# Kernel tuning notes

Hardware: AMD Instinct MI355X
Metric: run time of the kernel (lower is better)

Reference implementation:

```python
import jax, jax.numpy as jnp
import numpy as np

N = 50000        # nodes
E = 400000       # edges (avg degree 8)
F_IN = 128       # num_features
HID = 64         # hidden_channels
H = 4            # num_heads
D = HID // H     # headc = 16
C = 16           # num_classes
K_HOPS = 3
ALPHA = 0.1
CST = 1e-5


def setup_inputs() -> dict:
    key = jax.random.key(0)
    ks = jax.random.split(key, 16)
    s = 0.05
    x = jax.random.normal(ks[0], (N, F_IN), dtype=jnp.float32)
    edge_index = jax.random.randint(ks[1], (2, E), 0, N, dtype=jnp.int64)
    Wi = jax.random.normal(ks[2], (F_IN, HID), dtype=jnp.float32) * s
    bi = jnp.zeros((HID,), dtype=jnp.float32)
    Wq = jax.random.normal(ks[3], (HID, H * D), dtype=jnp.float32) * s
    bq = jnp.zeros((H * D,), dtype=jnp.float32)
    Wk = jax.random.normal(ks[4], (HID, H * D), dtype=jnp.float32) * s
    bk = jnp.zeros((H * D,), dtype=jnp.float32)
    Wv = jax.random.normal(ks[5], (HID, H * C), dtype=jnp.float32) * s
    bv = jnp.zeros((H * C,), dtype=jnp.float32)
    Wo = jax.random.normal(ks[6], (H * C, C), dtype=jnp.float32) * s
    bo = jnp.zeros((C,), dtype=jnp.float32)
    # hopwise/temp init as in the torch module (ind_gamma=True, gamma_softmax=True)
    hw = ALPHA * (1.0 - ALPHA) ** np.arange(K_HOPS + 1)
    hw[-1] = (1.0 - ALPHA) ** K_HOPS
    hopwise = jnp.asarray(hw, dtype=jnp.float32)
    temp = jax.random.uniform(ks[7], (H, K_HOPS + 1), dtype=jnp.float32)
    return {"x": x, "edge_index": edge_index, "Wi": Wi, "bi": bi, "Wq": Wq,
            "bq": bq, "Wk": Wk, "bk": bk, "Wv": Wv, "bv": bv, "Wo": Wo,
            "bo": bo, "hopwise": hopwise, "temp": temp}


def reference(x, edge_index, Wi, bi, Wq, bq, Wk, bk, Wv, bv, Wo, bo, hopwise, temp):
    # dropout p=0 (inference); input transform + relu
    h = jax.nn.relu(x @ Wi + bi)                       # (N, HID)
    Q = (1.0 + jax.nn.elu(h @ Wq + bq)).reshape(N, H, D)
    Kt = (1.0 + jax.nn.elu(h @ Wk + bk)).reshape(N, H, D)
    V = (h @ Wv + bv).reshape(N, H, C)
    M = jnp.einsum('nhi,nhj->nhij', Kt, V)             # (N, H, D, C)
    hidden = V * temp[:, 0][None, :, None]             # hop-0 term
    # NB: torch F.softmax(temp, dim=-2) normalizes over the HEAD axis
    layerwise = jax.nn.softmax(temp, axis=0)           # (H, K+1)
    src, dst = edge_index[0], edge_index[1]
    for hop in range(K_HOPS):
        M = jax.ops.segment_sum(M[src], dst, num_segments=N)
        Kt = jax.ops.segment_sum(Kt[src], dst, num_segments=N)
        Hm = jnp.einsum('nhi,nhij->nhj', Q, M)         # (N, H, C)
        den = jnp.einsum('nhi,nhi->nh', Q, Kt)[..., None] + CST
        gamma = hopwise[hop + 1] * layerwise[:, hop + 1][:, None]  # (H, 1)
        hidden = hidden + gamma * (Hm / den)
    # multi_concat=True path
    out = hidden.reshape(N, H * C) @ Wo + bo           # (N, C)
    return out
```

## Files before the change

kernel.cpp:

```cpp
#include <hip/hip_runtime.h>
#include <math.h>

#define F_IN 128
#define HID  64
#define NH   4
#define DD   16
#define CC   16
#define CSTE 1e-5f

typedef _Float16 h2     __attribute__((ext_vector_type(2)));
typedef float    f2     __attribute__((ext_vector_type(2)));
typedef short    short8 __attribute__((ext_vector_type(8)));
typedef float    f4v    __attribute__((ext_vector_type(4)));

#define WIT_LD 136
#define W2T_LD 72
#define H_LD   72

__device__ __forceinline__ unsigned short bf16r(float f) {
    unsigned int u = __builtin_bit_cast(unsigned int, f);
    unsigned int r = (u + 0x7FFFu + ((u >> 16) & 1u)) >> 16;
    return (unsigned short)r;
}

__device__ __forceinline__ float fp8_to_f32(unsigned int b) {
    f2 v = __builtin_amdgcn_cvt_pk_f32_fp8((int)b, false);
    return v.x;
}
__device__ __forceinline__ f2 fp8x2_to_f32(unsigned int w) {
    return __builtin_amdgcn_cvt_pk_f32_fp8((int)w, false);
}
__device__ __forceinline__ unsigned char f32_to_fp8(float f) {
    int w = __builtin_amdgcn_cvt_pk_fp8_f32(f, f, 0, false);
    return (unsigned char)(w & 0xff);
}

__device__ __forceinline__ float fp4_dec1(unsigned int n) {
    unsigned int e = (n >> 1) & 3u, m = n & 1u;
    float mag = (e == 0) ? 0.5f * (float)m
                         : (float)(1u << (e - 1)) * (1.0f + 0.5f * (float)m);
    return (n & 8u) ? -mag : mag;
}
__device__ __forceinline__ unsigned int fp4_enc1(float f) {
    unsigned int s = (f < 0.f) ? 8u : 0u;
    float a = fabsf(f);
    unsigned int m;
    if      (a < 0.25f) m = 0u;
    else if (a < 0.75f) m = 1u;
    else if (a < 1.25f) m = 2u;
    else if (a < 1.75f) m = 3u;
    else if (a < 2.5f)  m = 4u;
    else if (a < 3.5f)  m = 5u;
    else if (a < 5.0f)  m = 6u;
    else                m = 7u;
    return s | m;
}

#if __has_builtin(__builtin_amdgcn_cvt_scalef32_pk_f32_fp4) && __has_builtin(__builtin_amdgcn_cvt_scalef32_pk_fp4_f32)
#define HAS_FP4 1
#endif

__device__ __forceinline__ void fp4x16_dec(uint2 w, float* v) {
#ifdef HAS_FP4
    f2 r;
    r = __builtin_amdgcn_cvt_scalef32_pk_f32_fp4(w.x, 1.0f, 0); v[0]  = r.x; v[1]  = r.y;
    r = __builtin_amdgcn_cvt_scalef32_pk_f32_fp4(w.x, 1.0f, 1); v[2]  = r.x; v[3]  = r.y;
    r = __builtin_amdgcn_cvt_scalef32_pk_f32_fp4(w.x, 1.0f, 2); v[4]  = r.x; v[5]  = r.y;
    r = __builtin_amdgcn_cvt_scalef32_pk_f32_fp4(w.x, 1.0f, 3); v[6]  = r.x; v[7]  = r.y;
    r = __builtin_amdgcn_cvt_scalef32_pk_f32_fp4(w.y, 1.0f, 0); v[8]  = r.x; v[9]  = r.y;
    r = __builtin_amdgcn_cvt_scalef32_pk_f32_fp4(w.y, 1.0f, 1); v[10] = r.x; v[11] = r.y;
    r = __builtin_amdgcn_cvt_scalef32_pk_f32_fp4(w.y, 1.0f, 2); v[12] = r.x; v[13] = r.y;
    r = __builtin_amdgcn_cvt_scalef32_pk_f32_fp4(w.y, 1.0f, 3); v[14] = r.x; v[15] = r.y;
#else
    #pragma unroll
    for (int j = 0; j < 8; ++j) {
        v[j]     = fp4_dec1((w.x >> (4 * j)) & 0xFu);
        v[8 + j] = fp4_dec1((w.y >> (4 * j)) & 0xFu);
    }
#endif
}

__device__ __forceinline__ uint2 fp4x16_enc(const float* v) {
#ifdef HAS_FP4
    unsigned int a = 0u, b = 0u;
    a = __builtin_amdgcn_cvt_scalef32_pk_fp4_f32(a, v[0],  v[1],  1.0f, 0);
    a = __builtin_amdgcn_cvt_scalef32_pk_fp4_f32(a, v[2],  v[3],  1.0f, 1);
    a = __builtin_amdgcn_cvt_scalef32_pk_fp4_f32(a, v[4],  v[5],  1.0f, 2);
    a = __builtin_amdgcn_cvt_scalef32_pk_fp4_f32(a, v[6],  v[7],  1.0f, 3);
    b = __builtin_amdgcn_cvt_scalef32_pk_fp4_f32(b, v[8],  v[9],  1.0f, 0);
    b = __builtin_amdgcn_cvt_scalef32_pk_fp4_f32(b, v[10], v[11], 1.0f, 1);
    b = __builtin_amdgcn_cvt_scalef32_pk_fp4_f32(b, v[12], v[13], 1.0f, 2);
    b = __builtin_amdgcn_cvt_scalef32_pk_fp4_f32(b, v[14], v[15], 1.0f, 3);
    return {a, b};
#else
    unsigned int a = 0u, b = 0u;
    #pragma unroll
    for (int j = 0; j < 8; ++j) {
        a |= fp4_enc1(v[j])     << (4 * j);
        b |= fp4_enc1(v[8 + j]) << (4 * j);
    }
    return {a, b};
#endif
}

__device__ __forceinline__ void store_m_row(
    uint2* __restrict__ Mout, unsigned short* __restrict__ SKout,
    int node, int lane, const float* u, float kacc)
{
    float rm = 0.f;
    #pragma unroll
    for (int j = 0; j < 16; ++j) rm = fmaxf(rm, fabsf(u[j]));
    unsigned char s8 = f32_to_fp8(rm * (1.0f / 6.0f));
    float se = fp8_to_f32((unsigned int)s8);
    float invs = (se > 0.f) ? (1.0f / se) : 0.f;
    float tq[16];
    #pragma unroll
    for (int j = 0; j < 16; ++j) tq[j] = u[j] * invs;
    Mout[(size_t)node * 64 + lane] = fp4x16_enc(tq);
    SKout[(size_t)node * 64 + lane] =
        (unsigned short)((unsigned short)s8 | ((unsigned short)f32_to_fp8(kacc) << 8));
}

__device__ __forceinline__ float gamma_for(const float* __restrict__ temp,
                                           const float* __restrict__ hopwise,
                                           int h, int hop) {
    float t0 = temp[0 * 4 + hop], t1 = temp[1 * 4 + hop];
    float t2 = temp[2 * 4 + hop], t3 = temp[3 * 4 + hop];
    float mx = fmaxf(fmaxf(t0, t1), fmaxf(t2, t3));
    float e0 = __expf(t0 - mx), e1 = __expf(t1 - mx);
    float e2 = __expf(t2 - mx), e3 = __expf(t3 - mx);
    float ssum = e0 + e1 + e2 + e3;
    float eh = (h == 0) ? e0 : (h == 1) ? e1 : (h == 2) ? e2 : e3;
    return hopwise[hop] * eh / ssum;
}

__device__ __forceinline__ void reduce_scatter16(float* u, int p) {
    #pragma unroll
    for (int k = 0; k < 4; ++k) {
        const int m = 1 << k;
        bool bit = (p >> k) & 1;
        const int n = 8 >> k;
        #pragma unroll
        for (int j = 0; j < n; ++j) {
            float give = bit ? u[2 * j]     : u[2 * j + 1];
            float keep = bit ? u[2 * j + 1] : u[2 * j];
            float got  = __shfl_xor(give, m, 64);
            u[j] = keep + got;
        }
    }
}

__device__ __forceinline__ float den16(float qd, float kacc) {
    float kq = qd * kacc;
    kq += __shfl_xor(kq, 1, 64);
    kq += __shfl_xor(kq, 2, 64);
    kq += __shfl_xor(kq, 4, 64);
    kq += __shfl_xor(kq, 8, 64);
    return kq + CSTE;
}

__global__ __launch_bounds__(1024) void scan_a(const int* __restrict__ deg,
                                               int* __restrict__ offsets,
                                               int* __restrict__ bsum, int N) {
    __shared__ int wsum[16], woff[16];
    int lane = threadIdx.x & 63, w = threadIdx.x >> 6;
    int i0 = blockIdx.x * 4096 + (int)threadIdx.x * 4;
    int d0 = (i0 + 0 < N) ? deg[i0 + 0] : 0;
    int d1 = (i0 + 1 < N) ? deg[i0 + 1] : 0;
    int d2 = (i0 + 2 < N) ? deg[i0 + 2] : 0;
    int d3 = (i0 + 3 < N) ? deg[i0 + 3] : 0;
    int tsum = d0 + d1 + d2 + d3;
    int incl = tsum;
    #pragma unroll
    for (int m = 1; m < 64; m <<= 1) {
        int t = __shfl_up(incl, m, 64);
        if (lane >= m) incl += t;
    }
    if (lane == 63) wsum[w] = incl;
    __syncthreads();
    if (threadIdx.x == 0) {
        int r = 0;
        for (int k = 0; k < 16; ++k) { int t = wsum[k]; woff[k] = r; r += t; }
        bsum[blockIdx.x] = r;
    }
    __syncthreads();
    int excl = woff[w] + incl - tsum;
    if (i0 + 0 < N) offsets[i0 + 0] = excl;
    if (i0 + 1 < N) offsets[i0 + 1] = excl + d0;
    if (i0 + 2 < N) offsets[i0 + 2] = excl + d0 + d1;
    if (i0 + 3 < N) offsets[i0 + 3] = excl + d0 + d1 + d2;
}

__global__ void scan_c(int* __restrict__ offsets, const int* __restrict__ bsum,
                       int nb, int N) {
    int i = blockIdx.x * blockDim.x + threadIdx.x;
    if (i < N) {
        int bkt = i >> 12;
        int base = 0;
        for (int b = 0; b < bkt; ++b) base += bsum[b];
        offsets[i] += base;
    }
    if (i == 0) {
        int tot = 0;
        for (int b = 0; b < nb; ++b) tot += bsum[b];
        offsets[N] = tot;
    }
}

__global__ void scatter_kernel(const int* __restrict__ ei, const int* __restrict__ offsets,
                               int* __restrict__ cursor, int* __restrict__ csr, int E) {
    int e = blockIdx.x * blockDim.x + threadIdx.x;
    if (e < E) {
        int src = ei[e];
        int dst = ei[E + e];
        int pos = atomicAdd(&cursor[dst], 1);
        csr[offsets[dst] + pos] = src;
    }
}

__global__ __launch_bounds__(256) void qkv_count(
    const float* __restrict__ x,
    const float* __restrict__ Wi, const float* __restrict__ bi,
    const float* __restrict__ Wq, const float* __restrict__ bq,
    const float* __restrict__ Wk, const float* __restrict__ bk,
    const float* __restrict__ Wv, const float* __restrict__ bv,
    const float* __restrict__ temp,
    float* __restrict__ Q, unsigned char* __restrict__ K0,
    _Float16* __restrict__ Vh, float* __restrict__ hidden,
    const int* __restrict__ ei, int* __restrict__ deg,
    int E, int qb, int N)
{
    __shared__ unsigned short wit[64 * WIT_LD];
    __shared__ unsigned short w2t[192 * W2T_LD];
    __shared__ unsigned short hlds[64 * H_LD];
    if ((int)blockIdx.x >= qb) {
        int e = ((int)blockIdx.x - qb) * 256 + (int)threadIdx.x;
        if (e < E) atomicAdd(&deg[ei[E + e]], 1);
        return;
    }
    int t = threadIdx.x;
    #pragma unroll
    for (int i = 0; i < 32; ++i) {
        int g = t + i * 256;
        wit[(g & 63) * WIT_LD + (g >> 6)] = bf16r(Wi[g]);
    }
    #pragma unroll
    for (int i = 0; i < 16; ++i) {
        int g = t + i * 256;
        int k = g >> 6, n = g & 63;
        w2t[(n      ) * W2T_LD + k] = bf16r(Wq[g]);
        w2t[(n +  64) * W2T_LD + k] = bf16r(Wk[g]);
        w2t[(n + 128) * W2T_LD + k] = bf16r(Wv[g]);
    }
    __syncthreads();

    int lane = t & 63, w = t >> 6;
    int p = lane & 15, quad = lane >> 4;
    int mbase = blockIdx.x * 64 + w * 16;

    short8 afrag[4];
    {
        int node = mbase + p;
        if (node >= N) node = N - 1;
        const float* xr = x + (size_t)node * F_IN + quad * 8;
        #pragma unroll
        for (int ks = 0; ks < 4; ++ks) {
            float4 a0 = *(const float4*)(xr + ks * 32);
            float4 a1 = *(const float4*)(xr + ks * 32 + 4);
            short8 f;
            f[0] = bf16r(a0.x); f[1] = bf16r(a0.y); f[2] = bf16r(a0.z); f[3] = bf16r(a0.w);
            f[4] = bf16r(a1.x); f[5] = bf16r(a1.y); f[6] = bf16r(a1.z); f[7] = bf16r(a1.w);
            afrag[ks] = f;
        }
    }
    #pragma unroll
    for (int nt = 0; nt < 4; ++nt) {
        f4v acc = {0.f, 0.f, 0.f, 0.f};
        #pragma unroll
        for (int ks = 0; ks < 4; ++ks) {
            short8 b = *(const short8*)&wit[(nt * 16 + p) * WIT_LD + ks * 32 + quad * 8];
            acc = __builtin_amdgcn_mfma_f32_16x16x32_bf16(afrag[ks], b, acc, 0, 0, 0);
        }
        float bb = bi[nt * 16 + p];
        #pragma unroll
        for (int r = 0; r < 4; ++r) {
            float hv = fmaxf(acc[r] + bb, 0.f);
            hlds[(w * 16 + quad * 4 + r) * H_LD + nt * 16 + p] = bf16r(hv);
        }
    }
    __syncthreads();

    short8 ha0 = *(const short8*)&hlds[(w * 16 + p) * H_LD + quad * 8];
    short8 ha1 = *(const short8*)&hlds[(w * 16 + p) * H_LD + 32 + quad * 8];
    int node_r = mbase + quad * 4;
    #pragma unroll
    for (int nt = 0; nt < 12; ++nt) {
        f4v acc = {0.f, 0.f, 0.f, 0.f};
        short8 b0 = *(const short8*)&w2t[(nt * 16 + p) * W2T_LD + quad * 8];
        short8 b1 = *(const short8*)&w2t[(nt * 16 + p) * W2T_LD + 32 + quad * 8];
        acc = __builtin_amdgcn_mfma_f32_16x16x32_bf16(ha0, b0, acc, 0, 0, 0);
        acc = __builtin_amdgcn_mfma_f32_16x16x32_bf16(ha1, b1, acc, 0, 0, 0);
        int col = nt * 16 + p;
        #pragma unroll
        for (int r = 0; r < 4; ++r) {
            int node = node_r + r;
            if (node >= N) continue;
            float v = acc[r];
            if (col < 64) {
                v += bq[col];
                Q[(size_t)node * 64 + col] = (v > 0.f) ? (1.f + v) : __expf(v);
            } else if (col < 128) {
                int c = col - 64;
                v += bk[c];
                float kv = (v > 0.f) ? (1.f + v) : __expf(v);
                K0[(size_t)node * 64 + c] = f32_to_fp8(kv);
            } else {
                int c = col - 128;
                v += bv[c];
                Vh[(size_t)node * 64 + c] = (_Float16)v;
                hidden[(size_t)node * 64 + c] = v * temp[(c >> 4) * 4];
            }
        }
    }
}


__global__ __launch_bounds__(256) void hop1_all(
    const float* __restrict__ Q, const unsigned char* __restrict__ K0,
    const _Float16* __restrict__ Vh,
    const int* __restrict__ offsets, const int* __restrict__ csr,
    const float* __restrict__ temp, const float* __restrict__ hopwise,
    uint2* __restrict__ M1, unsigned short* __restrict__ SK1,
    float* __restrict__ hidden, int N)
{
    int lane = threadIdx.x & 63;
    int node = blockIdx.x * 4 + (threadIdx.x >> 6);
    if (node >= N) return;
    int h = lane >> 4;
    float gh = gamma_for(temp, hopwise, h, 1);
    h2 u16[8];
    #pragma unroll
    for (int j = 0; j < 8; ++j) u16[j] = h2{(_Float16)0.f, (_Float16)0.f};
    float kacc = 0.f;
    int beg = offsets[node], end = offsets[node + 1];
    int t = beg;
    for (; t + 1 < end; t += 2) {
        int s0 = csr[t], s1 = csr[t + 1];
        const uint4* v0p = (const uint4*)(Vh + (size_t)s0 * 64 + h * 16);
        const uint4* v1p = (const uint4*)(Vh + (size_t)s1 * 64 + h * 16);
        uint4 a0 = v0p[0], a1 = v0p[1];
        uint4 b0 = v1p[0], b1 = v1p[1];
        float k0 = fp8_to_f32(K0[(size_t)s0 * 64 + lane]);
        float k1 = fp8_to_f32(K0[(size_t)s1 * 64 + lane]);
        kacc += k0 + k1;
        _Float16 k0h = (_Float16)k0, k1h = (_Float16)k1;
        h2 k02 = {k0h, k0h}, k12 = {k1h, k1h};
        const unsigned int aw[8] = {a0.x, a0.y, a0.z, a0.w, a1.x, a1.y, a1.z, a1.w};
        const unsigned int bw[8] = {b0.x, b0.y, b0.z, b0.w, b1.x, b1.y, b1.z, b1.w};
        #pragma unroll
        for (int j = 0; j < 8; ++j) {
            u16[j] += k02 * __builtin_bit_cast(h2, aw[j]);
            u16[j] += k12 * __builtin_bit_cast(h2, bw[j]);
        }
    }
    for (; t < end; ++t) {
        int s = csr[t];
        const uint4* vp = (const uint4*)(Vh + (size_t)s * 64 + h * 16);
        uint4 a0 = vp[0], a1 = vp[1];
        float kk = fp8_to_f32(K0[(size_t)s * 64 + lane]);
        kacc += kk;
        _Float16 kh = (_Float16)kk;
        h2 k2 = {kh, kh};
        const unsigned int aw[8] = {a0.x, a0.y, a0.z, a0.w, a1.x, a1.y, a1.z, a1.w};
        #pragma unroll
        for (int j = 0; j < 8; ++j)
            u16[j] += k2 * __builtin_bit_cast(h2, aw[j]);
    }
    float u[16];
    #pragma unroll
    for (int j = 0; j < 8; ++j) { u[2 * j] = (float)u16[j].x; u[2 * j + 1] = (float)u16[j].y; }
    store_m_row(M1, SK1, node, lane, u, kacc);
    float qd = Q[(size_t)node * 64 + lane];
    #pragma unroll
    for (int j = 0; j < 16; ++j) u[j] *= qd;
    reduce_scatter16(u, lane & 15);
    float g = gh / den16(qd, kacc);
    hidden[(size_t)node * 64 + lane] += g * u[0];
}

template<bool STORE>
__global__ __launch_bounds__(256) void hop23_all(
    const float* __restrict__ Q, const uint2* __restrict__ Mprev,
    const unsigned short* __restrict__ SKprev,
    const int* __restrict__ offsets, const int* __restrict__ csr,
    const float* __restrict__ temp, const float* __restrict__ hopwise,
    uint2* __restrict__ Mnext, unsigned short* __restrict__ SKnext,
    float* __restrict__ hidden, int N, int hop)
{
    int lane = threadIdx.x & 63;
    int node = blockIdx.x * 4 + (threadIdx.x >> 6);
    if (node >= N) return;
    float gh = gamma_for(temp, hopwise, lane >> 4, hop);
    const uint2* Mb = Mprev + lane;
    const unsigned short* SKb = SKprev + lane;
    float u[16];
    #pragma unroll
    for (int j = 0; j < 16; ++j) u[j] = 0.f;
    float kacc = 0.f;
    int beg = offsets[node], end = offsets[node + 1];
    int t = beg;
    for (; t + 3 < end; t += 4) {
        int s0 = csr[t], s1 = csr[t + 1], s2 = csr[t + 2], s3 = csr[t + 3];
        uint2 w0 = Mb[(size_t)s0 * 64];
        uint2 w1 = Mb[(size_t)s1 * 64];
        uint2 w2 = Mb[(size_t)s2 * 64];
        uint2 w3 = Mb[(size_t)s3 * 64];
        f2 sk0 = fp8x2_to_f32(SKb[(size_t)s0 * 64]);
        f2 sk1 = fp8x2_to_f32(SKb[(size_t)s1 * 64]);
        f2 sk2 = fp8x2_to_f32(SKb[(size_t)s2 * 64]);
        f2 sk3 = fp8x2_to_f32(SKb[(size_t)s3 * 64]);
        kacc += (sk0.y + sk1.y) + (sk2.y + sk3.y);
        float v[16];
        fp4x16_dec(w0, v);
        #pragma unroll
        for (int j = 0; j < 16; ++j) u[j] = fmaf(sk0.x, v[j], u[j]);
        fp4x16_dec(w1, v);
        #pragma unroll
        for (int j = 0; j < 16; ++j) u[j] = fmaf(sk1.x, v[j], u[j]);
        fp4x16_dec(w2, v);
        #pragma unroll
        for (int j = 0; j < 16; ++j) u[j] = fmaf(sk2.x, v[j], u[j]);
        fp4x16_dec(w3, v);
        #pragma unroll
        for (int j = 0; j < 16; ++j) u[j] = fmaf(sk3.x, v[j], u[j]);
    }
    for (; t < end; ++t) {
        int sn = csr[t];
        uint2 w = Mb[(size_t)sn * 64];
        f2 sk = fp8x2_to_f32(SKb[(size_t)sn * 64]);
        kacc += sk.y;
        float v[16];
        fp4x16_dec(w, v);
        #pragma unroll
        for (int j = 0; j < 16; ++j) u[j] = fmaf(sk.x, v[j], u[j]);
    }
    if (STORE) store_m_row(Mnext, SKnext, node, lane, u, kacc);
    float qd = Q[(size_t)node * 64 + lane];
    #pragma unroll
    for (int j = 0; j < 16; ++j) u[j] *= qd;
    reduce_scatter16(u, lane & 15);
    float g = gh / den16(qd, kacc);
    hidden[(size_t)node * 64 + lane] += g * u[0];
}

__global__ __launch_bounds__(256) void out_kernel(
    const float* __restrict__ hidden, const float* __restrict__ Wo,
    const float* __restrict__ bo, float* __restrict__ out, int N)
{
    __shared__ float wo[HID * CC];
    for (int i = threadIdx.x; i < HID * CC; i += 256) wo[i] = Wo[i];
    __syncthreads();
    int idx = blockIdx.x * 256 + threadIdx.x;
    int n = idx >> 4, c = idx & 15;
    if (n >= N) return;
    float acc = bo[c];
    const float4* hp4 = (const float4*)(hidden + (size_t)n * HID);
    #pragma unroll
    for (int j4 = 0; j4 < 16; ++j4) {
        float4 hv = hp4[j4];
        acc += hv.x * wo[(4 * j4 + 0) * CC + c] + hv.y * wo[(4 * j4 + 1) * CC + c]
             + hv.z * wo[(4 * j4 + 2) * CC + c] + hv.w * wo[(4 * j4 + 3) * CC + c];
    }
    out[(size_t)n * CC + c] = acc;
}

extern "C" void kernel_launch(void* const* d_in, const int* in_sizes, int n_in,
                              void* d_out, int out_size, void* d_ws, size_t ws_size,
                              hipStream_t stream) {
    const float* x       = (const float*)d_in[0];
    const int*   ei      = (const int*)  d_in[1];
    const float* Wi      = (const float*)d_in[2];
    const float* bi      = (const float*)d_in[3];
    const float* Wq      = (const float*)d_in[4];
    const float* bq      = (const float*)d_in[5];
    const float* Wk      = (const float*)d_in[6];
    const float* bk      = (const float*)d_in[7];
    const float* Wv      = (const float*)d_in[8];
    const float* bv      = (const float*)d_in[9];
    const float* Wo      = (const float*)d_in[10];
    const float* bo      = (const float*)d_in[11];
    const float* hopwise = (const float*)d_in[12];
    const float* temp    = (const float*)d_in[13];

    const int N = in_sizes[0] / F_IN;
    const int E = in_sizes[1] / 2;

    char* ws = (char*)d_ws;
    size_t off = 0;
    auto take = [&](size_t bytes) -> char* {
        char* p = ws + off;
        off += (bytes + 255) & ~(size_t)255;
        return p;
    };
    float*          Q      = (float*)take((size_t)N * 64 * 4);
    _Float16*       Vh     = (_Float16*)take((size_t)N * 64 * 2);
    float*          hidden = (float*)take((size_t)N * 64 * 4);
    unsigned char*  K0     = (unsigned char*)take((size_t)N * 64);
    unsigned short* SK1    = (unsigned short*)take((size_t)N * 64 * 2);
    unsigned short* SK2    = (unsigned short*)take((size_t)N * 64 * 2);
    int*            degcur = (int*)take((size_t)2 * N * 4);
    int*            offs   = (int*)take((size_t)(N + 1) * 4);
    int*            csr    = (int*)take((size_t)E * 4);
    int             nb     = (N + 4095) / 4096;
    int*            bsum   = (int*)take((size_t)nb * 4);
    uint2*          M1     = (uint2*)take((size_t)N * 512);
    uint2*          M2     = (uint2*)take((size_t)N * 512);

    int* deg    = degcur;
    int* cursor = degcur + N;

    hipMemsetAsync(degcur, 0, (size_t)2 * N * 4, stream);

    int eb = (E + 255) / 256;
    int qb = (N + 63) / 64;
    qkv_count<<<qb + eb, 256, 0, stream>>>(x, Wi, bi, Wq, bq, Wk, bk, Wv, bv,
                                           temp, Q, K0, Vh, hidden,
                                           ei, deg, E, qb, N);
    scan_a<<<nb, 1024, 0, stream>>>(deg, offs, bsum, N);
    scan_c<<<(N + 255) / 256, 256, 0, stream>>>(offs, bsum, nb, N);
    scatter_kernel<<<eb, 256, 0, stream>>>(ei, offs, cursor, csr, E);

    int nb4 = (N + 3) / 4;
    hop1_all<<<nb4, 256, 0, stream>>>(Q, K0, Vh, offs, csr, temp, hopwise,
                                      M1, SK1, hidden, N);
    hop23_all<true ><<<nb4, 256, 0, stream>>>(Q, M1, SK1, offs, csr, temp, hopwise,
                                              M2, SK2, hidden, N, 2);
    hop23_all<false><<<nb4, 256, 0, stream>>>(Q, M2, SK2, offs, csr, temp, hopwise,
                                              (uint2*)nullptr, (unsigned short*)nullptr,
                                              hidden, N, 3);

    int ob = (N * CC + 255) / 256;
    out_kernel<<<ob, 256, 0, stream>>>(hidden, Wo, bo, (float*)d_out, N);
}
```

Baseline: 311.7 us.

## Fuse output projection into final hop and move hop-0 term into hop1

Removes the separate output-projection kernel by computing the hidden·Wo product inside the last hop kernel, using a per-lane Wo row and a cross-lane reduce. The hop-0 hidden initialization moves from the QKV kernel into hop1, which now writes hidden instead of read-modify-writing it. The hop2/3 inner accumulation switches to packed f32 FMA through inline asm, with paired fp4 decode. This saves one launch and several full passes over the hidden buffer, at the cost of more shuffles and registers in the final hop.

```diff
diff --git a/kernel.cpp b/kernel.cpp
--- a/kernel.cpp
+++ b/kernel.cpp
@@ -21,6 +21,11 @@
     unsigned int u = __builtin_bit_cast(unsigned int, f);
     unsigned int r = (u + 0x7FFFu + ((u >> 16) & 1u)) >> 16;
     return (unsigned short)r;
+}
+
+__device__ __forceinline__ f2 pk_fma(f2 a, f2 b, f2 c) {
+    asm("v_pk_fma_f32 %0, %1, %2, %0" : "+v"(c) : "v"(a), "v"(b));
+    return c;
 }
 
 __device__ __forceinline__ float fp8_to_f32(unsigned int b) {
@@ -60,22 +65,23 @@
 #define HAS_FP4 1
 #endif
 
-__device__ __forceinline__ void fp4x16_dec(uint2 w, float* v) {
+__device__ __forceinline__ void fp4x16_dec2(uint2 w, f2* v) {
 #ifdef HAS_FP4
-    f2 r;
-    r = __builtin_amdgcn_cvt_scalef32_pk_f32_fp4(w.x, 1.0f, 0); v[0]  = r.x; v[1]  = r.y;
-    r = __builtin_amdgcn_cvt_scalef32_pk_f32_fp4(w.x, 1.0f, 1); v[2]  = r.x; v[3]  = r.y;
-    r = __builtin_amdgcn_cvt_scalef32_pk_f32_fp4(w.x, 1.0f, 2); v[4]  = r.x; v[5]  = r.y;
-    r = __builtin_amdgcn_cvt_scalef32_pk_f32_fp4(w.x, 1.0f, 3); v[6]  = r.x; v[7]  = r.y;
-    r = __builtin_amdgcn_cvt_scalef32_pk_f32_fp4(w.y, 1.0f, 0); v[8]  = r.x; v[9]  = r.y;
-    r = __builtin_amdgcn_cvt_scalef32_pk_f32_fp4(w.y, 1.0f, 1); v[10] = r.x; v[11] = r.y;
-    r = __builtin_amdgcn_cvt_scalef32_pk_f32_fp4(w.y, 1.0f, 2); v[12] = r.x; v[13] = r.y;
-    r = __builtin_amdgcn_cvt_scalef32_pk_f32_fp4(w.y, 1.0f, 3); v[14] = r.x; v[15] = r.y;
+    v[0] = __builtin_amdgcn_cvt_scalef32_pk_f32_fp4(w.x, 1.0f, 0);
+    v[1] = __builtin_amdgcn_cvt_scalef32_pk_f32_fp4(w.x, 1.0f, 1);
+    v[2] = __builtin_amdgcn_cvt_scalef32_pk_f32_fp4(w.x, 1.0f, 2);
+    v[3] = __builtin_amdgcn_cvt_scalef32_pk_f32_fp4(w.x, 1.0f, 3);
+    v[4] = __builtin_amdgcn_cvt_scalef32_pk_f32_fp4(w.y, 1.0f, 0);
+    v[5] = __builtin_amdgcn_cvt_scalef32_pk_f32_fp4(w.y, 1.0f, 1);
+    v[6] = __builtin_amdgcn_cvt_scalef32_pk_f32_fp4(w.y, 1.0f, 2);
+    v[7] = __builtin_amdgcn_cvt_scalef32_pk_f32_fp4(w.y, 1.0f, 3);
 #else
     #pragma unroll
-    for (int j = 0; j < 8; ++j) {
-        v[j]     = fp4_dec1((w.x >> (4 * j)) & 0xFu);
-        v[8 + j] = fp4_dec1((w.y >> (4 * j)) & 0xFu);
+    for (int j = 0; j < 4; ++j) {
+        v[j].x     = fp4_dec1((w.x >> (8 * j)) & 0xFu);
+        v[j].y     = fp4_dec1((w.x >> (8 * j + 4)) & 0xFu);
+        v[4 + j].x = fp4_dec1((w.y >> (8 * j)) & 0xFu);
+        v[4 + j].y = fp4_dec1((w.y >> (8 * j + 4)) & 0xFu);
     }
 #endif
 }
@@ -224,9 +230,8 @@
     const float* __restrict__ Wq, const float* __restrict__ bq,
     const float* __restrict__ Wk, const float* __restrict__ bk,
     const float* __restrict__ Wv, const float* __restrict__ bv,
-    const float* __restrict__ temp,
     float* __restrict__ Q, unsigned char* __restrict__ K0,
-    _Float16* __restrict__ Vh, float* __restrict__ hidden,
+    _Float16* __restrict__ Vh,
     const int* __restrict__ ei, int* __restrict__ deg,
     int E, int qb, int N)
 {
@@ -318,7 +323,6 @@
                 int c = col - 128;
                 v += bv[c];
                 Vh[(size_t)node * 64 + c] = (_Float16)v;
-                hidden[(size_t)node * 64 + c] = v * temp[(c >> 4) * 4];
             }
         }
     }
@@ -338,6 +342,7 @@
     if (node >= N) return;
     int h = lane >> 4;
     float gh = gamma_for(temp, hopwise, h, 1);
+    float h0 = (float)Vh[(size_t)node * 64 + lane] * temp[h * 4];
     h2 u16[8];
     #pragma unroll
     for (int j = 0; j < 8; ++j) u16[j] = h2{(_Float16)0.f, (_Float16)0.f};
@@ -385,7 +390,7 @@
     for (int j = 0; j < 16; ++j) u[j] *= qd;
     reduce_scatter16(u, lane & 15);
     float g = gh / den16(qd, kacc);
-    hidden[(size_t)node * 64 + lane] += g * u[0];
+    hidden[(size_t)node * 64 + lane] = h0 + g * u[0];
 }
 
 template<bool STORE>
@@ -395,17 +400,28 @@
     const int* __restrict__ offsets, const int* __restrict__ csr,
     const float* __restrict__ temp, const float* __restrict__ hopwise,
     uint2* __restrict__ Mnext, unsigned short* __restrict__ SKnext,
-    float* __restrict__ hidden, int N, int hop)
+    float* __restrict__ hidden,
+    const float* __restrict__ Wo, const float* __restrict__ bo,
+    float* __restrict__ out, int N, int hop)
 {
     int lane = threadIdx.x & 63;
     int node = blockIdx.x * 4 + (threadIdx.x >> 6);
     if (node >= N) return;
     float gh = gamma_for(temp, hopwise, lane >> 4, hop);
+    float wrow[16];
+    if constexpr (!STORE) {
+        const f4v* wp = (const f4v*)(Wo + (size_t)lane * 16);
+        f4v a = wp[0], b = wp[1], c = wp[2], d = wp[3];
+        wrow[0]=a[0]; wrow[1]=a[1]; wrow[2]=a[2]; wrow[3]=a[3];
+        wrow[4]=b[0]; wrow[5]=b[1]; wrow[6]=b[2]; wrow[7]=b[3];
+        wrow[8]=c[0]; wrow[9]=c[1]; wrow[10]=c[2]; wrow[11]=c[3];
+        wrow[12]=d[0]; wrow[13]=d[1]; wrow[14]=d[2]; wrow[15]=d[3];
+    }
     const uint2* Mb = Mprev + lane;
     const unsigned short* SKb = SKprev + lane;
-    float u[16];
-    #pragma unroll
-    for (int j = 0; j < 16; ++j) u[j] = 0.f;
+    f2 u2[8];
+    #pragma unroll
+    for (int j = 0; j < 8; ++j) u2[j] = f2{0.f, 0.f};
     float kacc = 0.f;
     int beg = offsets[node], end = offsets[node + 1];
     int t = beg;
@@ -420,58 +436,58 @@
         f2 sk2 = fp8x2_to_f32(SKb[(size_t)s2 * 64]);
         f2 sk3 = fp8x2_to_f32(SKb[(size_t)s3 * 64]);
         kacc += (sk0.y + sk1.y) + (sk2.y + sk3.y);
-        float v[16];
-        fp4x16_dec(w0, v);
-        #pragma unroll
-        for (int j = 0; j < 16; ++j) u[j] = fmaf(sk0.x, v[j], u[j]);
-        fp4x16_dec(w1, v);
-        #pragma unroll
-        for (int j = 0; j < 16; ++j) u[j] = fmaf(sk1.x, v[j], u[j]);
-        fp4x16_dec(w2, v);
-        #pragma unroll
-        for (int j = 0; j < 16; ++j) u[j] = fmaf(sk2.x, v[j], u[j]);
-        fp4x16_dec(w3, v);
-        #pragma unroll
-        for (int j = 0; j < 16; ++j) u[j] = fmaf(sk3.x, v[j], u[j]);
+        f2 v[8];
+        f2 s;
+        fp4x16_dec2(w0, v);
+        s.x = sk0.x; s.y = sk0.x;
+        #pragma unroll
+        for (int j = 0; j < 8; ++j) u2[j] = pk_fma(s, v[j], u2[j]);
+        fp4x16_dec2(w1, v);
+        s.x = sk1.x; s.y = sk1.x;
+        #pragma unroll
+        for (int j = 0; j < 8; ++j) u2[j] = pk_fma(s, v[j], u2[j]);
+        fp4x16_dec2(w2, v);
+        s.x = sk2.x; s.y = sk2.x;
+        #pragma unroll
+        for (int j = 0; j < 8; ++j) u2[j] = pk_fma(s, v[j], u2[j]);
+        fp4x16_dec2(w3, v);
+        s.x = sk3.x; s.y = sk3.x;
+        #pragma unroll
+        for (int j = 0; j < 8; ++j) u2[j] = pk_fma(s, v[j], u2[j]);
     }
     for (; t < end; ++t) {
         int sn = csr[t];
         uint2 w = Mb[(size_t)sn * 64];
         f2 sk = fp8x2_to_f32(SKb[(size_t)sn * 64]);
         kacc += sk.y;
-        float v[16];
-        fp4x16_dec(w, v);
-        #pragma unroll
-        for (int j = 0; j < 16; ++j) u[j] = fmaf(sk.x, v[j], u[j]);
-    }
-    if (STORE) store_m_row(Mnext, SKnext, node, lane, u, kacc);
+        f2 v[8];
+        fp4x16_dec2(w, v);
+        f2 s; s.x = sk.x; s.y = sk.x;
+        #pragma unroll
+        for (int j = 0; j < 8; ++j) u2[j] = pk_fma(s, v[j], u2[j]);
+    }
+    float u[16];
+    #pragma unroll
+    for (int j = 0; j < 8; ++j) { u[2 * j] = u2[j].x; u[2 * j + 1] = u2[j].y; }
+    if constexpr (STORE) store_m_row(Mnext, SKnext, node, lane, u, kacc);
     float qd = Q[(size_t)node * 64 + lane];
     #pragma unroll
     for (int j = 0; j < 16; ++j) u[j] *= qd;
     reduce_scatter16(u, lane & 15);
     float g = gh / den16(qd, kacc);
-    hidden[(size_t)node * 64 + lane] += g * u[0];
-}
-
-__global__ __launch_bounds__(256) void out_kernel(
-    const float* __restrict__ hidden, const float* __restrict__ Wo,
-    const float* __restrict__ bo, float* __restrict__ out, int N)
-{
-    __shared__ float wo[HID * CC];
-    for (int i = threadIdx.x; i < HID * CC; i += 256) wo[i] = Wo[i];
-    __syncthreads();
-    int idx = blockIdx.x * 256 + threadIdx.x;
-    int n = idx >> 4, c = idx & 15;
-    if (n >= N) return;
-    float acc = bo[c];
-    const float4* hp4 = (const float4*)(hidden + (size_t)n * HID);
-    #pragma unroll
-    for (int j4 = 0; j4 < 16; ++j4) {
-        float4 hv = hp4[j4];
-        acc += hv.x * wo[(4 * j4 + 0) * CC + c] + hv.y * wo[(4 * j4 + 1) * CC + c]
-             + hv.z * wo[(4 * j4 + 2) * CC + c] + hv.w * wo[(4 * j4 + 3) * CC + c];
-    }
-    out[(size_t)n * CC + c] = acc;
+    if constexpr (STORE) {
+        hidden[(size_t)node * 64 + lane] += g * u[0];
+    } else {
+        float hv = hidden[(size_t)node * 64 + lane] + g * u[0];
+        float o[16];
+        #pragma unroll
+        for (int j = 0; j < 16; ++j) o[j] = hv * wrow[j];
+        reduce_scatter16(o, lane & 15);
+        float r = o[0];
+        r += __shfl_xor(r, 16, 64);
+        r += __shfl_xor(r, 32, 64);
+        if (lane < 16) out[(size_t)node * 16 + lane] = r + bo[lane];
+    }
 }
 
 extern "C" void kernel_launch(void* const* d_in, const int* in_sizes, int n_in,
@@ -524,7 +540,7 @@
     int eb = (E + 255) / 256;
     int qb = (N + 63) / 64;
     qkv_count<<<qb + eb, 256, 0, stream>>>(x, Wi, bi, Wq, bq, Wk, bk, Wv, bv,
-                                           temp, Q, K0, Vh, hidden,
+                                           Q, K0, Vh,
                                            ei, deg, E, qb, N);
     scan_a<<<nb, 1024, 0, stream>>>(deg, offs, bsum, N);
     scan_c<<<(N + 255) / 256, 256, 0, stream>>>(offs, bsum, nb, N);
@@ -534,11 +550,10 @@
     hop1_all<<<nb4, 256, 0, stream>>>(Q, K0, Vh, offs, csr, temp, hopwise,
                                       M1, SK1, hidden, N);
     hop23_all<true ><<<nb4, 256, 0, stream>>>(Q, M1, SK1, offs, csr, temp, hopwise,
-                                              M2, SK2, hidden, N, 2);
+                                              M2, SK2, hidden,
+                                              (const float*)nullptr, (const float*)nullptr,
+                                              (float*)nullptr, N, 2);
     hop23_all<false><<<nb4, 256, 0, stream>>>(Q, M2, SK2, offs, csr, temp, hopwise,
                                               (uint2*)nullptr, (unsigned short*)nullptr,
-                                              hidden, N, 3);
-
-    int ob = (N * CC + 255) / 256;
-    out_kernel<<<ob, 256, 0, stream>>>(hidden, Wo, bo, (float*)d_out, N);
-}
+                                              hidden, Wo, bo, (float*)d_out, N, 3);
+}
```

Result: slower. 328.2 us (+5.3%).
